# Optimization experiments

Hardware: AMD Instinct MI355X
Metric: run time of the kernel (lower is better)

The kernel has to match this reference:

```python
import jax, jax.numpy as jnp
import numpy as np

N_NODES = 50000
N_EDGES = 800000
F_IN = 64
H = 128
N_CLASSES = 10
NUM_GRAPHS = 512


def setup_inputs() -> dict:
    key = jax.random.key(0)
    ks = jax.random.split(key, 16)
    x = jax.random.normal(ks[0], (N_NODES, F_IN), dtype=jnp.float32)
    edge_index = jax.random.randint(ks[1], (2, N_EDGES), 0, N_NODES, dtype=jnp.int64)
    batch = jnp.sort(jax.random.randint(ks[2], (N_NODES,), 0, NUM_GRAPHS, dtype=jnp.int64))

    def lin(k, fi, fo):
        kw, kb = jax.random.split(k)
        s = 1.0 / np.sqrt(fi)
        return (jax.random.uniform(kw, (fi, fo), jnp.float32, -s, s),
                jax.random.uniform(kb, (fo,), jnp.float32, -s, s))

    W0, b0 = lin(ks[3], F_IN, H)
    W1, b1 = lin(ks[4], H, H)
    W2, b2 = lin(ks[5], H, H)
    mW0, mb0 = lin(ks[6], H, H)
    mW1, mb1 = lin(ks[7], H, H)
    mW2, mb2 = lin(ks[8], H, N_CLASSES)
    return {"x": x, "edge_index": edge_index, "batch": batch,
            "W0": W0, "b0": b0, "W1": W1, "b1": b1, "W2": W2, "b2": b2,
            "mW0": mW0, "mb0": mb0, "mW1": mW1, "mb1": mb1, "mW2": mW2, "mb2": mb2}


def reference(x, edge_index, batch, W0, b0, W1, b1, W2, b2, mW0, mb0, mW1, mb1, mW2, mb2):
    N = x.shape[0]
    loop = jnp.arange(N, dtype=edge_index.dtype)
    src = jnp.concatenate([edge_index[0], loop])  # add self-loops (PyG GCNConv)
    dst = jnp.concatenate([edge_index[1], loop])
    deg = jax.ops.segment_sum(jnp.ones_like(src, jnp.float32), dst, num_segments=N)
    dinv = jnp.where(deg > 0, deg ** -0.5, 0.0)
    norm = dinv[src] * dinv[dst]  # [E+N]

    def gcn(h, W, b):
        h = h @ W                                   # [N, H]
        msg = h[src] * norm[:, None]                # gather [E+N, H]
        return jax.ops.segment_sum(msg, dst, num_segments=N) + b

    h = jax.nn.relu(gcn(x, W0, b0))
    h = jax.nn.relu(gcn(h, W1, b1))
    h = jax.nn.relu(gcn(h, W2, b2))
    g = jax.ops.segment_sum(h, batch, num_segments=NUM_GRAPHS)  # global_add_pool
    g = jax.nn.relu(g @ mW0 + mb0)
    g = jax.nn.relu(g @ mW1 + mb1)
    return g @ mW2 + mb2  # [NUM_GRAPHS, N_CLASSES]
```

## Files before the change

### kernel.cpp

```cpp
#include <hip/hip_runtime.h>
#include <hip/hip_bf16.h>
#include <stdint.h>

#define N_NODES   50000
#define N_EDGES   800000
#define F_IN      64
#define HID       128
#define N_CLASSES 10
#define NUM_GRAPHS 512

#define NBUCK 128
#define BW    391
#define S1B   400
#define CHUNK 2000
#define MCNT  (NBUCK * S1B)
#define SCB   (MCNT / 256)
#define PREPB 3125
#define MAXB  8192

typedef unsigned int uint32;
typedef __attribute__((ext_vector_type(8))) short bf16x8;
typedef __attribute__((ext_vector_type(4))) float f32x4;

__device__ __forceinline__ float bl(uint32 w) { return __uint_as_float(w << 16); }
__device__ __forceinline__ float bh(uint32 w) { return __uint_as_float(w & 0xffff0000u); }
__device__ __forceinline__ float b1f(unsigned short h) { return __uint_as_float((uint32)h << 16); }
__device__ __forceinline__ uint32 packbf(float a, float b) {
    uint32 ua = __float_as_uint(a), ub = __float_as_uint(b);
    ua = (ua + 0x7fffu + ((ua >> 16) & 1u)) >> 16;
    ub = (ub + 0x7fffu + ((ub >> 16) & 1u)) >> 16;
    return ua | (ub << 16);
}
__device__ __forceinline__ unsigned short packbf1(float a) {
    uint32 ua = __float_as_uint(a);
    return (unsigned short)((ua + 0x7fffu + ((ua >> 16) & 1u)) >> 16);
}

__global__ __launch_bounds__(256) void prep_hist_kernel(const float4* __restrict__ x, uint2* __restrict__ xb,
                                                        const float* __restrict__ W0, unsigned short* __restrict__ W0t,
                                                        const float* __restrict__ W1, unsigned short* __restrict__ W1t,
                                                        const float* __restrict__ W2, unsigned short* __restrict__ W2t,
                                                        float* __restrict__ g,
                                                        const int* __restrict__ dst, int* __restrict__ bcnt, int E) {
    __shared__ int cnt[NBUCK];
    int blk = blockIdx.x;
    int t = threadIdx.x;
    if (blk < PREPB) {
        int i = blk * 256 + t;
        if (i < N_NODES * F_IN / 4) {
            float4 v = x[i];
            xb[i] = make_uint2(packbf(v.x, v.y), packbf(v.z, v.w));
        }
        if (i < NUM_GRAPHS * HID) g[i] = 0.f;
        if (i < 64 * 128) {
            int k = i >> 7, j = i & 127;
            W0t[j * (64 + 8) + k] = packbf1(W0[i]);
        }
        int i2 = i - 64 * 128;
        if (i2 >= 0 && i2 < 128 * 128) {
            int k = i2 >> 7, j = i2 & 127;
            W1t[j * (128 + 8) + k] = packbf1(W1[i2]);
            W2t[j * (128 + 8) + k] = packbf1(W2[i2]);
        }
    } else {
        int b2 = blk - PREPB;
        if (t < NBUCK) cnt[t] = 0;
        __syncthreads();
        int base = b2 * CHUNK;
        for (int i = t; i < CHUNK; i += 256) {
            int e = base + i;
            if (e < E) atomicAdd(&cnt[(uint32)dst[e] / BW], 1);
        }
        __syncthreads();
        if (t < NBUCK) bcnt[t * S1B + b2] = cnt[t];
    }
}

__global__ __launch_bounds__(256) void scanA_kernel(const int* __restrict__ in,
                                                    int* __restrict__ incl,
                                                    int* __restrict__ bsum_raw, int M) {
    __shared__ int s[256];
    int t = threadIdx.x;
    int i = blockIdx.x * 256 + t;
    int v = (i < M) ? in[i] : 0;
    s[t] = v;
    __syncthreads();
    #pragma unroll
    for (int d = 1; d < 256; d <<= 1) {
        int a = (t >= d) ? s[t - d] : 0;
        __syncthreads();
        s[t] += a;
        __syncthreads();
    }
    if (i < M) incl[i] = s[t];
    if (t == 255) bsum_raw[blockIdx.x] = s[255];
}

__device__ __forceinline__ void local_top_scan(const int* __restrict__ bsum_raw, int* exs, int t) {
    int bv = (t < SCB) ? bsum_raw[t] : 0;
    exs[t] = bv;
    __syncthreads();
    #pragma unroll
    for (int d = 1; d < 256; d <<= 1) {
        int a = (t >= d) ? exs[t - d] : 0;
        __syncthreads();
        exs[t] += a;
        __syncthreads();
    }
    int iv = exs[t];
    __syncthreads();
    exs[t] = iv - bv;
    __syncthreads();
}

__global__ __launch_bounds__(256) void bscatter_kernel(const int* __restrict__ src,
                                                       const int* __restrict__ dst,
                                                       const int* __restrict__ incl,
                                                       const int* __restrict__ bsum_raw,
                                                       uint32* __restrict__ ebuf, int E) {
    __shared__ int exs[256];
    __shared__ int cnt[NBUCK];
    __shared__ int cur[NBUCK];
    int t = threadIdx.x, blk = blockIdx.x;

    local_top_scan(bsum_raw, exs, t);

    if (t < NBUCK) cnt[t] = 0;
    __syncthreads();
    int base = blk * CHUNK;
    for (int i = t; i < CHUNK; i += 256) {
        int e = base + i;
        if (e < E) atomicAdd(&cnt[(uint32)dst[e] / BW], 1);
    }
    __syncthreads();
    if (t < NBUCK) {
        int idx = t * S1B + blk;
        cur[t] = exs[idx >> 8] + incl[idx] - cnt[t];
    }
    __syncthreads();
    for (int i = t; i < CHUNK; i += 256) {
        int e = base + i;
        if (e < E) {
            int d = dst[e];
            int slot = atomicAdd(&cur[(uint32)d / BW], 1);
            ebuf[slot] = (uint32)src[e] | ((uint32)d << 16);
        }
    }
}

__global__ __launch_bounds__(256) void bfinal_kernel(const uint32* __restrict__ ebuf,
                                                     const int* __restrict__ bcnt,
                                                     const int* __restrict__ incl,
                                                     const int* __restrict__ bsum_raw,
                                                     int2* __restrict__ rowse,
                                                     float* __restrict__ dinv,
                                                     uint32* __restrict__ meta, int E, int N) {
    __shared__ int exs[256];
    __shared__ int cnt[392];
    __shared__ int startv[400];
    __shared__ int segt[16];
    __shared__ uint32 smeta[MAXB];
    int t = threadIdx.x, b = blockIdx.x;

    local_top_scan(bsum_raw, exs, t);

    int bs, be;
    {
        int idx = b * S1B;
        bs = exs[idx >> 8] + incl[idx] - bcnt[idx];
        if (b + 1 >= NBUCK) be = E;
        else {
            int idx1 = (b + 1) * S1B;
            be = exs[idx1 >> 8] + incl[idx1] - bcnt[idx1];
        }
    }
    int sz = be - bs;

    for (int i = t; i < 392; i += 256) cnt[i] = 0;
    __syncthreads();
    for (int i = bs + t; i < be; i += 256) {
        uint32 d = ebuf[i] >> 16;
        atomicAdd(&cnt[d - b * BW], 1);
    }
    __syncthreads();

    if (t < 16) {
        int run = 0;
        #pragma unroll
        for (int k = 0; k < 25; k++) {
            int idx = t * 25 + k;
            int c = (idx < 391) ? cnt[idx] : 0;
            startv[idx] = run;
            run += c;
        }
        segt[t] = run;
    }
    __syncthreads();
    if (t == 0) {
        int run = 0;
        #pragma unroll
        for (int j = 0; j < 16; j++) { int s = segt[j]; segt[j] = run; run += s; }
    }
    __syncthreads();
    for (int l = t; l < 391; l += 256) startv[l] += segt[l / 25];
    __syncthreads();

    int locN = N - b * BW; if (locN > BW) locN = BW;
    for (int l = t; l < locN; l += 256) {
        int gn = b * BW + l;
        int st = bs + startv[l];
        rowse[gn] = make_int2(st, st + cnt[l]);
        dinv[gn] = rsqrtf((float)(cnt[l] + 1));
    }
    __syncthreads();

    if (sz <= MAXB) {
        for (int i = bs + t; i < be; i += 256) {
            uint32 v = ebuf[i];
            int slot = atomicAdd(&startv[(v >> 16) - b * BW], 1);
            smeta[slot] = v;
        }
        __syncthreads();
        for (int i = t; i < sz; i += 256) meta[bs + i] = smeta[i];
    } else {
        for (int i = bs + t; i < be; i += 256) {
            uint32 v = ebuf[i];
            int slot = atomicAdd(&startv[(v >> 16) - b * BW], 1);
            meta[bs + slot] = v;
        }
    }
}

__global__ __launch_bounds__(256) void spmm64_kernel(const int2* __restrict__ rowse,
                                                     uint32* __restrict__ meta,
                                                     const float* __restrict__ dinv,
                                                     const unsigned short* __restrict__ Hin,
                                                     unsigned short* __restrict__ Hout, int N) {
    int wave = threadIdx.x >> 6;
    int lane = threadIdx.x & 63;
    int node = blockIdx.x * 4 + wave;
    if (node >= N) return;
    int oct = lane >> 3;
    int sub = lane & 7;

    const uint4* Hv = (const uint4*)Hin;
    float di = dinv[node];
    float sn = di * di;

    float acc[8];
    if (oct == 0) {
        uint4 s = Hv[(size_t)node * 8 + sub];
        acc[0] = sn * bl(s.x); acc[1] = sn * bh(s.x);
        acc[2] = sn * bl(s.y); acc[3] = sn * bh(s.y);
        acc[4] = sn * bl(s.z); acc[5] = sn * bh(s.z);
        acc[6] = sn * bl(s.w); acc[7] = sn * bh(s.w);
    } else {
        #pragma unroll
        for (int v = 0; v < 8; v++) acc[v] = 0.f;
    }

    int2 se = rowse[node];
    int e0 = se.x, e1 = se.y;
    for (int e = e0; e < e1; e += 16) {
        int i0 = e + oct;
        int i1 = e + 8 + oct;
        bool v0 = i0 < e1, v1 = i1 < e1;
        uint32 m0 = v0 ? meta[i0] : 0u;
        uint32 m1 = v1 ? meta[i1] : 0u;
        uint32 s0 = m0 & 0xffffu, s1 = m1 & 0xffffu;
        float n0 = v0 ? di * dinv[s0] : 0.f;
        float n1 = v1 ? di * dinv[s1] : 0.f;
        if (sub == 0) {
            if (v0) meta[i0] = s0 | ((uint32)packbf1(n0) << 16);
            if (v1) meta[i1] = s1 | ((uint32)packbf1(n1) << 16);
        }
        uint4 r0 = Hv[(size_t)s0 * 8 + sub];
        uint4 r1 = Hv[(size_t)s1 * 8 + sub];
        acc[0] = fmaf(n0, bl(r0.x), acc[0]); acc[1] = fmaf(n0, bh(r0.x), acc[1]);
        acc[2] = fmaf(n0, bl(r0.y), acc[2]); acc[3] = fmaf(n0, bh(r0.y), acc[3]);
        acc[4] = fmaf(n0, bl(r0.z), acc[4]); acc[5] = fmaf(n0, bh(r0.z), acc[5]);
        acc[6] = fmaf(n0, bl(r0.w), acc[6]); acc[7] = fmaf(n0, bh(r0.w), acc[7]);
        acc[0] = fmaf(n1, bl(r1.x), acc[0]); acc[1] = fmaf(n1, bh(r1.x), acc[1]);
        acc[2] = fmaf(n1, bl(r1.y), acc[2]); acc[3] = fmaf(n1, bh(r1.y), acc[3]);
        acc[4] = fmaf(n1, bl(r1.z), acc[4]); acc[5] = fmaf(n1, bh(r1.z), acc[5]);
        acc[6] = fmaf(n1, bl(r1.w), acc[6]); acc[7] = fmaf(n1, bh(r1.w), acc[7]);
    }

    #pragma unroll
    for (int v = 0; v < 8; v++) {
        acc[v] += __shfl_xor(acc[v], 8);
        acc[v] += __shfl_xor(acc[v], 16);
        acc[v] += __shfl_xor(acc[v], 32);
    }

    if (oct == 0) {
        uint4 o;
        o.x = packbf(acc[0], acc[1]);
        o.y = packbf(acc[2], acc[3]);
        o.z = packbf(acc[4], acc[5]);
        o.w = packbf(acc[6], acc[7]);
        ((uint4*)Hout)[(size_t)node * 8 + sub] = o;
    }
}

__global__ __launch_bounds__(256) void spmm128_kernel(const int2* __restrict__ rowse,
                                                      const uint32* __restrict__ meta,
                                                      const float* __restrict__ dinv,
                                                      const unsigned short* __restrict__ Hin,
                                                      unsigned short* __restrict__ Hout, int N) {
    int wave = threadIdx.x >> 6;
    int lane = threadIdx.x & 63;
    int node = blockIdx.x * 4 + wave;
    if (node >= N) return;
    int q   = lane >> 4;
    int sub = lane & 15;

    const uint4* Hv = (const uint4*)Hin;
    float di = dinv[node];
    float sn = di * di;

    float acc[8];
    if (q == 0) {
        uint4 s = Hv[(size_t)node * 16 + sub];
        acc[0] = sn * bl(s.x); acc[1] = sn * bh(s.x);
        acc[2] = sn * bl(s.y); acc[3] = sn * bh(s.y);
        acc[4] = sn * bl(s.z); acc[5] = sn * bh(s.z);
        acc[6] = sn * bl(s.w); acc[7] = sn * bh(s.w);
    } else {
        #pragma unroll
        for (int v = 0; v < 8; v++) acc[v] = 0.f;
    }

    int2 se = rowse[node];
    int e0 = se.x, e1 = se.y;
    for (int e = e0; e < e1; e += 16) {
        int i0 = e + q;
        int i1 = e + 4 + q;
        int i2 = e + 8 + q;
        int i3 = e + 12 + q;
        uint32 m0 = (i0 < e1) ? meta[i0] : 0u;
        uint32 m1 = (i1 < e1) ? meta[i1] : 0u;
        uint32 m2 = (i2 < e1) ? meta[i2] : 0u;
        uint32 m3 = (i3 < e1) ? meta[i3] : 0u;
        float n0 = bh(m0);
        float n1 = bh(m1);
        float n2 = bh(m2);
        float n3 = bh(m3);
        uint4 r0 = Hv[(size_t)(m0 & 0xffffu) * 16 + sub];
        uint4 r1 = Hv[(size_t)(m1 & 0xffffu) * 16 + sub];
        uint4 r2 = Hv[(size_t)(m2 & 0xffffu) * 16 + sub];
        uint4 r3 = Hv[(size_t)(m3 & 0xffffu) * 16 + sub];
        acc[0] = fmaf(n0, bl(r0.x), acc[0]); acc[1] = fmaf(n0, bh(r0.x), acc[1]);
        acc[2] = fmaf(n0, bl(r0.y), acc[2]); acc[3] = fmaf(n0, bh(r0.y), acc[3]);
        acc[4] = fmaf(n0, bl(r0.z), acc[4]); acc[5] = fmaf(n0, bh(r0.z), acc[5]);
        acc[6] = fmaf(n0, bl(r0.w), acc[6]); acc[7] = fmaf(n0, bh(r0.w), acc[7]);
        acc[0] = fmaf(n1, bl(r1.x), acc[0]); acc[1] = fmaf(n1, bh(r1.x), acc[1]);
        acc[2] = fmaf(n1, bl(r1.y), acc[2]); acc[3] = fmaf(n1, bh(r1.y), acc[3]);
        acc[4] = fmaf(n1, bl(r1.z), acc[4]); acc[5] = fmaf(n1, bh(r1.z), acc[5]);
        acc[6] = fmaf(n1, bl(r1.w), acc[6]); acc[7] = fmaf(n1, bh(r1.w), acc[7]);
        acc[0] = fmaf(n2, bl(r2.x), acc[0]); acc[1] = fmaf(n2, bh(r2.x), acc[1]);
        acc[2] = fmaf(n2, bl(r2.y), acc[2]); acc[3] = fmaf(n2, bh(r2.y), acc[3]);
        acc[4] = fmaf(n2, bl(r2.z), acc[4]); acc[5] = fmaf(n2, bh(r2.z), acc[5]);
        acc[6] = fmaf(n2, bl(r2.w), acc[6]); acc[7] = fmaf(n2, bh(r2.w), acc[7]);
        acc[0] = fmaf(n3, bl(r3.x), acc[0]); acc[1] = fmaf(n3, bh(r3.x), acc[1]);
        acc[2] = fmaf(n3, bl(r3.y), acc[2]); acc[3] = fmaf(n3, bh(r3.y), acc[3]);
        acc[4] = fmaf(n3, bl(r3.z), acc[4]); acc[5] = fmaf(n3, bh(r3.z), acc[5]);
        acc[6] = fmaf(n3, bl(r3.w), acc[6]); acc[7] = fmaf(n3, bh(r3.w), acc[7]);
    }

    #pragma unroll
    for (int v = 0; v < 8; v++) {
        acc[v] += __shfl_xor(acc[v], 16);
        acc[v] += __shfl_xor(acc[v], 32);
    }

    if (q == 0) {
        uint4 o;
        o.x = packbf(acc[0], acc[1]);
        o.y = packbf(acc[2], acc[3]);
        o.z = packbf(acc[4], acc[5]);
        o.w = packbf(acc[6], acc[7]);
        ((uint4*)Hout)[(size_t)node * 16 + sub] = o;
    }
}

template <int K, bool POOL>
__global__ __launch_bounds__(256) void gemm_mfma_kernel(const unsigned short* __restrict__ A,
                                                        const unsigned short* __restrict__ Wt,
                                                        const float* __restrict__ bias,
                                                        unsigned short* __restrict__ out,
                                                        const int* __restrict__ batch,
                                                        float* __restrict__ g,
                                                        int N) {
    constexpr int KP = K + 8;
    __shared__ unsigned short Wl[128 * KP];
    __shared__ unsigned short Hl[POOL ? 128 * 128 : 1];

    int t = threadIdx.x;
    constexpr int TOT = 128 * KP * 2 / 16;
    #pragma unroll
    for (int i = 0; i < (TOT + 255) / 256; i++) {
        int idx = i * 256 + t;
        if (idx < TOT) ((uint4*)Wl)[idx] = ((const uint4*)Wt)[idx];
    }
    __syncthreads();

    int wave = t >> 6;
    int lane = t & 63;
    int rowBase = blockIdx.x * 128 + wave * 32;
    int r0 = rowBase + (lane & 15);
    int r1 = r0 + 16;
    if (r0 >= N) r0 = N - 1;
    if (r1 >= N) r1 = N - 1;
    int kchunk = lane >> 4;
    int colSub = lane & 15;

    f32x4 acc0[8], acc1[8];
    #pragma unroll
    for (int i = 0; i < 8; i++) { acc0[i] = (f32x4)0.0f; acc1[i] = (f32x4)0.0f; }

    #pragma unroll
    for (int s = 0; s < K / 32; s++) {
        bf16x8 a0 = *(const bf16x8*)(A + (size_t)r0 * K + s * 32 + kchunk * 8);
        bf16x8 a1 = *(const bf16x8*)(A + (size_t)r1 * K + s * 32 + kchunk * 8);
        #pragma unroll
        for (int tl = 0; tl < 8; tl++) {
            bf16x8 b = *(const bf16x8*)(Wl + (tl * 16 + colSub) * KP + s * 32 + kchunk * 8);
            acc0[tl] = __builtin_amdgcn_mfma_f32_16x16x32_bf16(a0, b, acc0[tl], 0, 0, 0);
            acc1[tl] = __builtin_amdgcn_mfma_f32_16x16x32_bf16(a1, b, acc1[tl], 0, 0, 0);
        }
    }

    int rowOff = (lane >> 4) * 4;
    if (!POOL) {
        #pragma unroll
        for (int tl = 0; tl < 8; tl++) {
            int col = tl * 16 + colSub;
            float bv = bias[col];
            #pragma unroll
            for (int r = 0; r < 4; r++) {
                int rowA = rowBase + rowOff + r;
                int rowB = rowA + 16;
                if (rowA < N) {
                    float v = fmaxf(acc0[tl][r] + bv, 0.f);
                    out[(size_t)rowA * 128 + col] = packbf1(v);
                }
                if (rowB < N) {
                    float v = fmaxf(acc1[tl][r] + bv, 0.f);
                    out[(size_t)rowB * 128 + col] = packbf1(v);
                }
            }
        }
    } else {
        int blockBase = blockIdx.x * 128;
        #pragma unroll
        for (int tl = 0; tl < 8; tl++) {
            int col = tl * 16 + colSub;
            float bv = bias[col];
            #pragma unroll
            for (int r = 0; r < 4; r++) {
                int lrA = wave * 32 + rowOff + r;
                int lrB = lrA + 16;
                Hl[lrA * 128 + col] = packbf1(fmaxf(acc0[tl][r] + bv, 0.f));
                Hl[lrB * 128 + col] = packbf1(fmaxf(acc1[tl][r] + bv, 0.f));
            }
        }
        __syncthreads();
        if (t < 128) {
            int limit = N - blockBase; if (limit > 128) limit = 128;
            float s = 0.f;
            int gid = batch[blockBase];
            for (int r = 0; r < limit; r++) {
                int bg = batch[blockBase + r];
                if (bg != gid) {
                    atomicAdd(&g[gid * HID + t], s);
                    s = 0.f;
                    gid = bg;
                }
                s += b1f(Hl[r * 128 + t]);
            }
            atomicAdd(&g[gid * HID + t], s);
        }
    }
}

__global__ __launch_bounds__(128) void mlp_kernel(const float* __restrict__ g,
                                                  const float* __restrict__ mW0, const float* __restrict__ mb0,
                                                  const float* __restrict__ mW1, const float* __restrict__ mb1,
                                                  const float* __restrict__ mW2, const float* __restrict__ mb2,
                                                  float* __restrict__ out) {
    int b = blockIdx.x;
    int j = threadIdx.x;
    __shared__ float l0[HID];
    __shared__ float l1[HID];
    l0[j] = g[b * HID + j];
    __syncthreads();

    {
        float a0 = mb0[j], a1 = 0.f, a2 = 0.f, a3 = 0.f;
        #pragma unroll 4
        for (int k = 0; k < HID; k += 4) {
            a0 = fmaf(l0[k + 0], mW0[(k + 0) * HID + j], a0);
            a1 = fmaf(l0[k + 1], mW0[(k + 1) * HID + j], a1);
            a2 = fmaf(l0[k + 2], mW0[(k + 2) * HID + j], a2);
            a3 = fmaf(l0[k + 3], mW0[(k + 3) * HID + j], a3);
        }
        l1[j] = fmaxf((a0 + a1) + (a2 + a3), 0.f);
    }
    __syncthreads();

    float c;
    {
        float a0 = mb1[j], a1 = 0.f, a2 = 0.f, a3 = 0.f;
        #pragma unroll 4
        for (int k = 0; k < HID; k += 4) {
            a0 = fmaf(l1[k + 0], mW1[(k + 0) * HID + j], a0);
            a1 = fmaf(l1[k + 1], mW1[(k + 1) * HID + j], a1);
            a2 = fmaf(l1[k + 2], mW1[(k + 2) * HID + j], a2);
            a3 = fmaf(l1[k + 3], mW1[(k + 3) * HID + j], a3);
        }
        c = fmaxf((a0 + a1) + (a2 + a3), 0.f);
    }
    __syncthreads();
    l0[j] = c;
    __syncthreads();

    if (j < N_CLASSES) {
        float a0 = mb2[j], a1 = 0.f, a2 = 0.f, a3 = 0.f;
        #pragma unroll 4
        for (int k = 0; k < HID; k += 4) {
            a0 = fmaf(l0[k + 0], mW2[(k + 0) * N_CLASSES + j], a0);
            a1 = fmaf(l0[k + 1], mW2[(k + 1) * N_CLASSES + j], a1);
            a2 = fmaf(l0[k + 2], mW2[(k + 2) * N_CLASSES + j], a2);
            a3 = fmaf(l0[k + 3], mW2[(k + 3) * N_CLASSES + j], a3);
        }
        out[b * N_CLASSES + j] = (a0 + a1) + (a2 + a3);
    }
}

extern "C" void kernel_launch(void* const* d_in, const int* in_sizes, int n_in,
                              void* d_out, int out_size, void* d_ws, size_t ws_size,
                              hipStream_t stream) {
    const float* x     = (const float*)d_in[0];
    const int*   ei    = (const int*)d_in[1];
    const int*   batch = (const int*)d_in[2];
    const float* W0  = (const float*)d_in[3];
    const float* b0  = (const float*)d_in[4];
    const float* W1  = (const float*)d_in[5];
    const float* b1  = (const float*)d_in[6];
    const float* W2  = (const float*)d_in[7];
    const float* b2  = (const float*)d_in[8];
    const float* mW0 = (const float*)d_in[9];
    const float* mb0 = (const float*)d_in[10];
    const float* mW1 = (const float*)d_in[11];
    const float* mb1 = (const float*)d_in[12];
    const float* mW2 = (const float*)d_in[13];
    const float* mb2 = (const float*)d_in[14];
    float* out = (float*)d_out;

    const int N = N_NODES, E = N_EDGES;
    const int* src = ei;
    const int* dst = ei + E;

    char* w = (char*)d_ws;
    auto alloc = [&](size_t bytes) -> void* {
        void* p = (void*)w;
        w += (bytes + 255) & ~(size_t)255;
        return p;
    };
    int2*   rowse    = (int2*)alloc((size_t)N * 8);
    uint32* ebuf     = (uint32*)alloc((size_t)E * 4);
    uint32* meta     = (uint32*)alloc((size_t)E * 4);
    int*    bcnt     = (int*)alloc((size_t)MCNT * 4);
    int*    incl     = (int*)alloc((size_t)MCNT * 4);
    int*    bsum_raw = (int*)alloc(256 * 4);
    float*  dinv     = (float*)alloc((size_t)N * 4);
    float*  g        = (float*)alloc((size_t)NUM_GRAPHS * HID * 4);
    unsigned short* xb   = (unsigned short*)alloc((size_t)N * F_IN * 2);
    unsigned short* bufA = (unsigned short*)alloc((size_t)N * HID * 2);
    unsigned short* bufB = (unsigned short*)alloc((size_t)N * HID * 2);
    unsigned short* W0t  = (unsigned short*)alloc((size_t)128 * (64 + 8) * 2);
    unsigned short* W1t  = (unsigned short*)alloc((size_t)128 * (128 + 8) * 2);
    unsigned short* W2t  = (unsigned short*)alloc((size_t)128 * (128 + 8) * 2);

    const int SPB  = (N + 3) / 4;
    const int GB   = (N + 127) / 128;

    prep_hist_kernel<<<PREPB + S1B, 256, 0, stream>>>((const float4*)x, (uint2*)xb,
                                                      W0, W0t, W1, W1t, W2, W2t, g,
                                                      dst, bcnt, E);
    scanA_kernel<<<SCB, 256, 0, stream>>>(bcnt, incl, bsum_raw, MCNT);
    bscatter_kernel<<<S1B, 256, 0, stream>>>(src, dst, incl, bsum_raw, ebuf, E);
    bfinal_kernel<<<NBUCK, 256, 0, stream>>>(ebuf, bcnt, incl, bsum_raw, rowse, dinv, meta, E, N);

    spmm64_kernel<<<SPB, 256, 0, stream>>>(rowse, meta, dinv, xb, bufA, N);
    gemm_mfma_kernel<64, false><<<GB, 256, 0, stream>>>(bufA, W0t, b0, bufB, batch, g, N);

    spmm128_kernel<<<SPB, 256, 0, stream>>>(rowse, meta, dinv, bufB, bufA, N);
    gemm_mfma_kernel<128, false><<<GB, 256, 0, stream>>>(bufA, W1t, b1, bufB, batch, g, N);

    spmm128_kernel<<<SPB, 256, 0, stream>>>(rowse, meta, dinv, bufB, bufA, N);
    gemm_mfma_kernel<128, true><<<GB, 256, 0, stream>>>(bufA, W2t, b2, bufB, batch, g, N);

    mlp_kernel<<<NUM_GRAPHS, 128, 0, stream>>>(g, mW0, mb0, mW1, mb1, mW2, mb2, out);
}
```

Before: 186.0 us.

## Quantize hidden activations to per-row uint8 for sparse aggregation gathers

The GEMM epilogue now writes the post-ReLU hidden features as uint8 with a per-row scale instead of bf16, and the 128-wide SpMM reads these 8-bit rows. Halving the bytes per gathered row cuts the memory traffic of the random neighbour gathers that dominate aggregation. To match the new column order of the aggregated output, the W1/W2 transposes are permuted. The cost is an extra scale lookup per edge and a loss of precision from 8-bit quantization, which may exceed the accuracy tolerance.

```diff
diff --git a/kernel.cpp b/kernel.cpp
--- a/kernel.cpp
+++ b/kernel.cpp
@@ -35,6 +35,7 @@
     uint32 ua = __float_as_uint(a);
     return (unsigned short)((ua + 0x7fffu + ((ua >> 16) & 1u)) >> 16);
 }
+
 
 __global__ __launch_bounds__(256) void prep_hist_kernel(const float4* __restrict__ x, uint2* __restrict__ xb,
                                                         const float* __restrict__ W0, unsigned short* __restrict__ W0t,
@@ -59,8 +60,9 @@
         int i2 = i - 64 * 128;
         if (i2 >= 0 && i2 < 128 * 128) {
             int k = i2 >> 7, j = i2 & 127;
-            W1t[j * (128 + 8) + k] = packbf1(W1[i2]);
-            W2t[j * (128 + 8) + k] = packbf1(W2[i2]);
+            int kp = (k & 15) * 8 + (k >> 4);
+            W1t[j * (128 + 8) + kp] = packbf1(W1[i2]);
+            W2t[j * (128 + 8) + kp] = packbf1(W2[i2]);
         }
     } else {
         int b2 = blk - PREPB;
@@ -303,84 +305,73 @@
     }
 }
 
-__global__ __launch_bounds__(256) void spmm128_kernel(const int2* __restrict__ rowse,
-                                                      const uint32* __restrict__ meta,
-                                                      const float* __restrict__ dinv,
-                                                      const unsigned short* __restrict__ Hin,
-                                                      unsigned short* __restrict__ Hout, int N) {
+__device__ __forceinline__ void fma16_u8(uint4 u, float ns, float* acc) {
+    #pragma unroll
+    for (int w = 0; w < 4; w++) {
+        uint32 xv = (&u.x)[w];
+        acc[w * 4 + 0] = fmaf(ns, (float)(xv & 255u),         acc[w * 4 + 0]);
+        acc[w * 4 + 1] = fmaf(ns, (float)((xv >> 8) & 255u),  acc[w * 4 + 1]);
+        acc[w * 4 + 2] = fmaf(ns, (float)((xv >> 16) & 255u), acc[w * 4 + 2]);
+        acc[w * 4 + 3] = fmaf(ns, (float)(xv >> 24),          acc[w * 4 + 3]);
+    }
+}
+
+__global__ __launch_bounds__(256) void spmm128q_kernel(const int2* __restrict__ rowse,
+                                                       const uint32* __restrict__ meta,
+                                                       const float* __restrict__ dinv,
+                                                       const unsigned char* __restrict__ Hq,
+                                                       const float* __restrict__ scale,
+                                                       unsigned short* __restrict__ Hout, int N) {
     int wave = threadIdx.x >> 6;
     int lane = threadIdx.x & 63;
     int node = blockIdx.x * 4 + wave;
     if (node >= N) return;
-    int q   = lane >> 4;
-    int sub = lane & 15;
-
-    const uint4* Hv = (const uint4*)Hin;
+    int oct = lane >> 3;
+    int sub = lane & 7;
+
+    const uint4* Hv = (const uint4*)Hq;
     float di = dinv[node];
     float sn = di * di;
 
-    float acc[8];
-    if (q == 0) {
-        uint4 s = Hv[(size_t)node * 16 + sub];
-        acc[0] = sn * bl(s.x); acc[1] = sn * bh(s.x);
-        acc[2] = sn * bl(s.y); acc[3] = sn * bh(s.y);
-        acc[4] = sn * bl(s.z); acc[5] = sn * bh(s.z);
-        acc[6] = sn * bl(s.w); acc[7] = sn * bh(s.w);
-    } else {
-        #pragma unroll
-        for (int v = 0; v < 8; v++) acc[v] = 0.f;
+    float acc[16];
+    #pragma unroll
+    for (int v = 0; v < 16; v++) acc[v] = 0.f;
+    if (oct == 0) {
+        uint4 u = Hv[(size_t)node * 8 + sub];
+        float ss = sn * scale[node];
+        fma16_u8(u, ss, acc);
     }
 
     int2 se = rowse[node];
     int e0 = se.x, e1 = se.y;
     for (int e = e0; e < e1; e += 16) {
-        int i0 = e + q;
-        int i1 = e + 4 + q;
-        int i2 = e + 8 + q;
-        int i3 = e + 12 + q;
+        int i0 = e + oct;
+        int i1 = e + 8 + oct;
         uint32 m0 = (i0 < e1) ? meta[i0] : 0u;
         uint32 m1 = (i1 < e1) ? meta[i1] : 0u;
-        uint32 m2 = (i2 < e1) ? meta[i2] : 0u;
-        uint32 m3 = (i3 < e1) ? meta[i3] : 0u;
-        float n0 = bh(m0);
-        float n1 = bh(m1);
-        float n2 = bh(m2);
-        float n3 = bh(m3);
-        uint4 r0 = Hv[(size_t)(m0 & 0xffffu) * 16 + sub];
-        uint4 r1 = Hv[(size_t)(m1 & 0xffffu) * 16 + sub];
-        uint4 r2 = Hv[(size_t)(m2 & 0xffffu) * 16 + sub];
-        uint4 r3 = Hv[(size_t)(m3 & 0xffffu) * 16 + sub];
-        acc[0] = fmaf(n0, bl(r0.x), acc[0]); acc[1] = fmaf(n0, bh(r0.x), acc[1]);
-        acc[2] = fmaf(n0, bl(r0.y), acc[2]); acc[3] = fmaf(n0, bh(r0.y), acc[3]);
-        acc[4] = fmaf(n0, bl(r0.z), acc[4]); acc[5] = fmaf(n0, bh(r0.z), acc[5]);
-        acc[6] = fmaf(n0, bl(r0.w), acc[6]); acc[7] = fmaf(n0, bh(r0.w), acc[7]);
-        acc[0] = fmaf(n1, bl(r1.x), acc[0]); acc[1] = fmaf(n1, bh(r1.x), acc[1]);
-        acc[2] = fmaf(n1, bl(r1.y), acc[2]); acc[3] = fmaf(n1, bh(r1.y), acc[3]);
-        acc[4] = fmaf(n1, bl(r1.z), acc[4]); acc[5] = fmaf(n1, bh(r1.z), acc[5]);
-        acc[6] = fmaf(n1, bl(r1.w), acc[6]); acc[7] = fmaf(n1, bh(r1.w), acc[7]);
-        acc[0] = fmaf(n2, bl(r2.x), acc[0]); acc[1] = fmaf(n2, bh(r2.x), acc[1]);
-        acc[2] = fmaf(n2, bl(r2.y), acc[2]); acc[3] = fmaf(n2, bh(r2.y), acc[3]);
-        acc[4] = fmaf(n2, bl(r2.z), acc[4]); acc[5] = fmaf(n2, bh(r2.z), acc[5]);
-        acc[6] = fmaf(n2, bl(r2.w), acc[6]); acc[7] = fmaf(n2, bh(r2.w), acc[7]);
-        acc[0] = fmaf(n3, bl(r3.x), acc[0]); acc[1] = fmaf(n3, bh(r3.x), acc[1]);
-        acc[2] = fmaf(n3, bl(r3.y), acc[2]); acc[3] = fmaf(n3, bh(r3.y), acc[3]);
-        acc[4] = fmaf(n3, bl(r3.z), acc[4]); acc[5] = fmaf(n3, bh(r3.z), acc[5]);
-        acc[6] = fmaf(n3, bl(r3.w), acc[6]); acc[7] = fmaf(n3, bh(r3.w), acc[7]);
-    }
-
-    #pragma unroll
-    for (int v = 0; v < 8; v++) {
+        uint32 s0 = m0 & 0xffffu, s1 = m1 & 0xffffu;
+        float ns0 = bh(m0) * scale[s0];
+        float ns1 = bh(m1) * scale[s1];
+        uint4 u0 = Hv[(size_t)s0 * 8 + sub];
+        uint4 u1 = Hv[(size_t)s1 * 8 + sub];
+        fma16_u8(u0, ns0, acc);
+        fma16_u8(u1, ns1, acc);
+    }
+
+    #pragma unroll
+    for (int v = 0; v < 16; v++) {
+        acc[v] += __shfl_xor(acc[v], 8);
         acc[v] += __shfl_xor(acc[v], 16);
         acc[v] += __shfl_xor(acc[v], 32);
     }
 
-    if (q == 0) {
-        uint4 o;
-        o.x = packbf(acc[0], acc[1]);
-        o.y = packbf(acc[2], acc[3]);
-        o.z = packbf(acc[4], acc[5]);
-        o.w = packbf(acc[6], acc[7]);
-        ((uint4*)Hout)[(size_t)node * 16 + sub] = o;
+    if (oct == 0) {
+        uint32 o[8];
+        #pragma unroll
+        for (int i = 0; i < 8; i++) o[i] = packbf(acc[2 * i], acc[2 * i + 1]);
+        uint4* dst = (uint4*)(Hout + (size_t)node * 128) + sub * 2;
+        dst[0] = make_uint4(o[0], o[1], o[2], o[3]);
+        dst[1] = make_uint4(o[4], o[5], o[6], o[7]);
     }
 }
 
@@ -388,7 +379,8 @@
 __global__ __launch_bounds__(256) void gemm_mfma_kernel(const unsigned short* __restrict__ A,
                                                         const unsigned short* __restrict__ Wt,
                                                         const float* __restrict__ bias,
-                                                        unsigned short* __restrict__ out,
+                                                        unsigned char* __restrict__ Hq,
+                                                        float* __restrict__ scale,
                                                         const int* __restrict__ batch,
                                                         float* __restrict__ g,
                                                         int N) {
@@ -433,24 +425,38 @@
 
     int rowOff = (lane >> 4) * 4;
     if (!POOL) {
-        #pragma unroll
-        for (int tl = 0; tl < 8; tl++) {
-            int col = tl * 16 + colSub;
-            float bv = bias[col];
+        auto quant_rows = [&](f32x4 (&ac)[8], int rbase) {
             #pragma unroll
             for (int r = 0; r < 4; r++) {
-                int rowA = rowBase + rowOff + r;
-                int rowB = rowA + 16;
-                if (rowA < N) {
-                    float v = fmaxf(acc0[tl][r] + bv, 0.f);
-                    out[(size_t)rowA * 128 + col] = packbf1(v);
+                int row = rbase + r;
+                float v[8];
+                float m = 0.f;
+                #pragma unroll
+                for (int tl = 0; tl < 8; tl++) {
+                    float tv = fmaxf(ac[tl][r] + bias[tl * 16 + colSub], 0.f);
+                    v[tl] = tv;
+                    m = fmaxf(m, tv);
                 }
-                if (rowB < N) {
-                    float v = fmaxf(acc1[tl][r] + bv, 0.f);
-                    out[(size_t)rowB * 128 + col] = packbf1(v);
+                m = fmaxf(m, __shfl_xor(m, 1));
+                m = fmaxf(m, __shfl_xor(m, 2));
+                m = fmaxf(m, __shfl_xor(m, 4));
+                m = fmaxf(m, __shfl_xor(m, 8));
+                float inv = (m > 0.f) ? 255.f / m : 0.f;
+                if (row < N) {
+                    uint32 b0 = 0, b1 = 0;
+                    #pragma unroll
+                    for (int tl = 0; tl < 4; tl++)
+                        b0 |= ((uint32)fmaf(v[tl], inv, 0.5f)) << (8 * tl);
+                    #pragma unroll
+                    for (int tl = 4; tl < 8; tl++)
+                        b1 |= ((uint32)fmaf(v[tl], inv, 0.5f)) << (8 * (tl - 4));
+                    ((uint2*)(Hq + (size_t)row * 128))[colSub] = make_uint2(b0, b1);
+                    if (colSub == 0) scale[row] = m * (1.f / 255.f);
                 }
             }
-        }
+        };
+        quant_rows(acc0, rowBase + rowOff);
+        quant_rows(acc1, rowBase + rowOff + 16);
     } else {
         int blockBase = blockIdx.x * 128;
         #pragma unroll
@@ -576,15 +582,16 @@
     int*    bsum_raw = (int*)alloc(256 * 4);
     float*  dinv     = (float*)alloc((size_t)N * 4);
     float*  g        = (float*)alloc((size_t)NUM_GRAPHS * HID * 4);
-    unsigned short* xb   = (unsigned short*)alloc((size_t)N * F_IN * 2);
-    unsigned short* bufA = (unsigned short*)alloc((size_t)N * HID * 2);
-    unsigned short* bufB = (unsigned short*)alloc((size_t)N * HID * 2);
-    unsigned short* W0t  = (unsigned short*)alloc((size_t)128 * (64 + 8) * 2);
-    unsigned short* W1t  = (unsigned short*)alloc((size_t)128 * (128 + 8) * 2);
-    unsigned short* W2t  = (unsigned short*)alloc((size_t)128 * (128 + 8) * 2);
-
-    const int SPB  = (N + 3) / 4;
-    const int GB   = (N + 127) / 128;
+    float*  scale    = (float*)alloc((size_t)N * 4);
+    unsigned char*  Hq  = (unsigned char*)alloc((size_t)N * 128);
+    unsigned short* xb  = (unsigned short*)alloc((size_t)N * F_IN * 2);
+    unsigned short* agg = (unsigned short*)alloc((size_t)N * HID * 2);
+    unsigned short* W0t = (unsigned short*)alloc((size_t)128 * (64 + 8) * 2);
+    unsigned short* W1t = (unsigned short*)alloc((size_t)128 * (128 + 8) * 2);
+    unsigned short* W2t = (unsigned short*)alloc((size_t)128 * (128 + 8) * 2);
+
+    const int SPB = (N + 3) / 4;
+    const int GB  = (N + 127) / 128;
 
     prep_hist_kernel<<<PREPB + S1B, 256, 0, stream>>>((const float4*)x, (uint2*)xb,
                                                       W0, W0t, W1, W1t, W2, W2t, g,
@@ -593,14 +600,14 @@
     bscatter_kernel<<<S1B, 256, 0, stream>>>(src, dst, incl, bsum_raw, ebuf, E);
     bfinal_kernel<<<NBUCK, 256, 0, stream>>>(ebuf, bcnt, incl, bsum_raw, rowse, dinv, meta, E, N);
 
-    spmm64_kernel<<<SPB, 256, 0, stream>>>(rowse, meta, dinv, xb, bufA, N);
-    gemm_mfma_kernel<64, false><<<GB, 256, 0, stream>>>(bufA, W0t, b0, bufB, batch, g, N);
-
-    spmm128_kernel<<<SPB, 256, 0, stream>>>(rowse, meta, dinv, bufB, bufA, N);
-    gemm_mfma_kernel<128, false><<<GB, 256, 0, stream>>>(bufA, W1t, b1, bufB, batch, g, N);
-
-    spmm128_kernel<<<SPB, 256, 0, stream>>>(rowse, meta, dinv, bufB, bufA, N);
-    gemm_mfma_kernel<128, true><<<GB, 256, 0, stream>>>(bufA, W2t, b2, bufB, batch, g, N);
+    spmm64_kernel<<<SPB, 256, 0, stream>>>(rowse, meta, dinv, xb, agg, N);
+    gemm_mfma_kernel<64, false><<<GB, 256, 0, stream>>>(agg, W0t, b0, Hq, scale, batch, g, N);
+
+    spmm128q_kernel<<<SPB, 256, 0, stream>>>(rowse, meta, dinv, Hq, scale, agg, N);
+    gemm_mfma_kernel<128, false><<<GB, 256, 0, stream>>>(agg, W1t, b1, Hq, scale, batch, g, N);
+
+    spmm128q_kernel<<<SPB, 256, 0, stream>>>(rowse, meta, dinv, Hq, scale, agg, N);
+    gemm_mfma_kernel<128, true><<<GB, 256, 0, stream>>>(agg, W2t, b2, Hq, scale, batch, g, N);
 
     mlp_kernel<<<NUM_GRAPHS, 128, 0, stream>>>(g, mW0, mb0, mW1, mb1, mW2, mb2, out);
 }
```

Measured after the change: 177.8 us (median of 3 runs). -4.4%, faster.
